# Performance work log

Measured on AMD Instinct MI355X. Metric: run time of the kernel, lower is better.

Reference implementation:

```python
import jax, jax.numpy as jnp
import numpy as np
import math

D_MODEL = 1024
NUM_HEADS = 16
HEAD_DIM = D_MODEL // NUM_HEADS
BATCH = 2
SEQ = 2048
THETA = 10000.0


def _rope_tables(seq_len, head_dim, theta=THETA):
    inv_freq = 1.0 / theta ** (jnp.arange(0, head_dim, 2, dtype=jnp.float32) / head_dim)
    pos = jnp.arange(seq_len, dtype=jnp.float32)
    freqs = jnp.outer(pos, inv_freq)                 # [S, hd/2]
    emb = jnp.concatenate([freqs, freqs], axis=-1)   # [S, hd]
    return jnp.cos(emb), jnp.sin(emb)


def _rotate_half(x):
    x1, x2 = jnp.split(x, 2, axis=-1)
    return jnp.concatenate([-x2, x1], axis=-1)


def setup_inputs() -> dict:
    key = jax.random.key(0)
    k1, k2, k3 = jax.random.split(key, 3)
    x = jax.random.normal(k1, (BATCH, SEQ, D_MODEL), dtype=jnp.float32)
    # causal mask: 1 where attend allowed, 0 where masked
    mask = jnp.tril(jnp.ones((SEQ, SEQ), dtype=jnp.int32))[None, None]
    w_qkv = jax.random.normal(k2, (D_MODEL, 3 * D_MODEL), dtype=jnp.float32) / math.sqrt(D_MODEL)
    w_out = jax.random.normal(k3, (D_MODEL, D_MODEL), dtype=jnp.float32) / math.sqrt(D_MODEL)
    return {"x": x, "mask": mask, "w_qkv": w_qkv, "w_out": w_out}


def reference(x, mask, w_qkv, w_out):
    B, S, _ = x.shape
    qkv = x @ w_qkv                                          # [B,S,3*D]
    qkv = qkv.reshape(B, S, 3, NUM_HEADS, HEAD_DIM)
    qkv = jnp.transpose(qkv, (2, 0, 3, 1, 4))                # [3,B,H,S,hd]
    q, k, v = qkv[0], qkv[1], qkv[2]
    cos, sin = _rope_tables(S, HEAD_DIM)                     # [S,hd]
    cos = cos[None, None]; sin = sin[None, None]
    q = q * cos + _rotate_half(q) * sin
    k = k * cos + _rotate_half(k) * sin
    scores = jnp.einsum('bhqd,bhkd->bhqk', q, k) / math.sqrt(HEAD_DIM)
    scores = jnp.where(mask == 0, -jnp.inf, scores)
    attn = jax.nn.softmax(scores, axis=-1)                   # dropout p=0 (eval)
    out = jnp.einsum('bhqk,bhkd->bhqd', attn, v)             # [B,H,S,hd]
    out = jnp.transpose(out, (0, 2, 1, 3)).reshape(B, S, D_MODEL)
    return out @ w_out
```

## Files before the change

kernel.cpp:

```cpp
#include <hip/hip_runtime.h>

typedef __bf16 bf16;
typedef __bf16 bf16x4 __attribute__((ext_vector_type(4)));
typedef __bf16 bf16x8 __attribute__((ext_vector_type(8)));
typedef short s16x4 __attribute__((ext_vector_type(4)));
typedef float f32x4 __attribute__((ext_vector_type(4)));

constexpr int BATCH = 2;
constexpr int SEQ   = 2048;
constexpr int DMODEL= 1024;
constexpr int NH    = 16;
constexpr int HD    = 64;
constexpr int M_ROWS= BATCH * SEQ;
constexpr int N_QKV = 3 * DMODEL;

__device__ __forceinline__ void gl_lds16(const bf16* g, bf16* l) {
  __builtin_amdgcn_global_load_lds(
      (const __attribute__((address_space(1))) unsigned int*)g,
      (__attribute__((address_space(3))) unsigned int*)l, 16, 0, 0);
}

__device__ __forceinline__ f32x4 mfma_16x16x16_bf16(bf16x4 a, bf16x4 b,
                                                    f32x4 c) {
#if defined(__HIP_DEVICE_COMPILE__)
  union { bf16x4 h; s16x4 s; } ua{a}, ub{b};
  return __builtin_amdgcn_mfma_f32_16x16x16bf16_1k(ua.s, ub.s, c, 0, 0, 0);
#else
  return c;
#endif
}

__global__ __launch_bounds__(256) void transpose_cast_kernel(
    const float* __restrict__ src, bf16* __restrict__ dst, int R, int C) {
  __shared__ float tile[32][33];
  const int c0 = blockIdx.x * 32, r0 = blockIdx.y * 32;
  const int tx = threadIdx.x, ty = threadIdx.y;
#pragma unroll
  for (int i = 0; i < 4; i++)
    tile[ty + 8 * i][tx] = src[(size_t)(r0 + ty + 8 * i) * C + c0 + tx];
  __syncthreads();
#pragma unroll
  for (int i = 0; i < 4; i++)
    dst[(size_t)(c0 + ty + 8 * i) * R + r0 + tx] = (bf16)tile[tx][ty + 8 * i];
}

__global__ __launch_bounds__(256) void cast_f32_bf16(
    const float* __restrict__ src, bf16* __restrict__ dst) {
  const int i = (blockIdx.x * 256 + threadIdx.x) * 8;
  float4 f0 = *(const float4*)&src[i];
  float4 f1 = *(const float4*)&src[i + 4];
  bf16x8 v;
  v[0] = (bf16)f0.x; v[1] = (bf16)f0.y; v[2] = (bf16)f0.z; v[3] = (bf16)f0.w;
  v[4] = (bf16)f1.x; v[5] = (bf16)f1.y; v[6] = (bf16)f1.z; v[7] = (bf16)f1.w;
  *(bf16x8*)&dst[i] = v;
}

#define GEMM_BODY(A, BT, K)                                                    \
  __shared__ bf16 As[128 * 32];                                                \
  __shared__ bf16 Bs[128 * 32];                                                \
  const int t = threadIdx.x;                                                   \
  const int m0 = blockIdx.y * 128;                                             \
  const int n0 = blockIdx.x * 128;                                             \
  const int w = t >> 6, lane = t & 63, g = lane >> 4, li = lane & 15;          \
  const int r0w = (w & 1) * 64, c0w = (w >> 1) * 64;                           \
  f32x4 acc[4][4] = {};                                                        \
  for (int k0 = 0; k0 < (K); k0 += 32) {                                       \
    __syncthreads();                                                           \
    _Pragma("unroll") for (int c = 0; c < 2; c++) {                            \
      const int idx = (w * 2 + c) * 64 + lane;                                 \
      const int row = idx >> 2, col = (idx & 3) * 8;                           \
      gl_lds16(&(A)[(size_t)(m0 + row) * (K) + k0 + col],                      \
               &As[(w * 2 + c) * 512]);                                        \
      gl_lds16(&(BT)[(size_t)(n0 + row) * (K) + k0 + col],                     \
               &Bs[(w * 2 + c) * 512]);                                        \
    }                                                                          \
    __syncthreads();                                                           \
    bf16x8 a[4], b[4];                                                         \
    _Pragma("unroll") for (int mt = 0; mt < 4; mt++)                           \
        a[mt] = *(const bf16x8*)&As[(r0w + mt * 16 + li) * 32 + g * 8];        \
    _Pragma("unroll") for (int nt = 0; nt < 4; nt++)                           \
        b[nt] = *(const bf16x8*)&Bs[(c0w + nt * 16 + li) * 32 + g * 8];        \
    _Pragma("unroll") for (int mt = 0; mt < 4; mt++)                           \
        _Pragma("unroll") for (int nt = 0; nt < 4; nt++)                       \
            acc[mt][nt] = __builtin_amdgcn_mfma_f32_16x16x32_bf16(             \
                a[mt], b[nt], acc[mt][nt], 0, 0, 0);                           \
  }

__global__ __launch_bounds__(256) void gemm_out64(
    const bf16* __restrict__ A, const bf16* __restrict__ BT,
    float* __restrict__ C, int M, int N, int K) {
  __shared__ bf16 As[64 * 32];
  __shared__ bf16 Bs[128 * 32];
  const int t = threadIdx.x;
  const int m0 = blockIdx.y * 64;
  const int n0 = blockIdx.x * 128;
  const int w = t >> 6, lane = t & 63, g = lane >> 4, li = lane & 15;
  const int r0w = (w & 1) * 32, c0w = (w >> 1) * 64;
  f32x4 acc[2][4] = {};
  for (int k0 = 0; k0 < K; k0 += 32) {
    __syncthreads();
    {
      const int idx = w * 64 + lane;
      const int row = idx >> 2, col = (idx & 3) * 8;
      gl_lds16(&A[(size_t)(m0 + row) * K + k0 + col], &As[w * 512]);
    }
#pragma unroll
    for (int c = 0; c < 2; c++) {
      const int idx = (w * 2 + c) * 64 + lane;
      const int row = idx >> 2, col = (idx & 3) * 8;
      gl_lds16(&BT[(size_t)(n0 + row) * K + k0 + col], &Bs[(w * 2 + c) * 512]);
    }
    __syncthreads();
    bf16x8 a[2], b[4];
#pragma unroll
    for (int mt = 0; mt < 2; mt++)
      a[mt] = *(const bf16x8*)&As[(r0w + mt * 16 + li) * 32 + g * 8];
#pragma unroll
    for (int nt = 0; nt < 4; nt++)
      b[nt] = *(const bf16x8*)&Bs[(c0w + nt * 16 + li) * 32 + g * 8];
#pragma unroll
    for (int mt = 0; mt < 2; mt++)
#pragma unroll
      for (int nt = 0; nt < 4; nt++)
        acc[mt][nt] = __builtin_amdgcn_mfma_f32_16x16x32_bf16(
            a[mt], b[nt], acc[mt][nt], 0, 0, 0);
  }
#pragma unroll
  for (int mt = 0; mt < 2; mt++)
#pragma unroll
    for (int nt = 0; nt < 4; nt++)
#pragma unroll
      for (int r = 0; r < 4; r++) {
        const int m = m0 + r0w + mt * 16 + g * 4 + r;
        const int n = n0 + c0w + nt * 16 + li;
        C[(size_t)m * N + n] = acc[mt][nt][r];
      }
}

__global__ __launch_bounds__(256) void gemm_qkv_rope(
    const bf16* __restrict__ A, const bf16* __restrict__ BT,
    bf16* __restrict__ Qb, bf16* __restrict__ Kb, bf16* __restrict__ Vt) {
  constexpr int K = DMODEL;
  GEMM_BODY(A, BT, K)

  const int region = n0 >> 10;
  const int b = m0 >> 11;
  const int h = ((n0 + c0w) >> 6) & 15;
  const size_t bh = (size_t)(b * NH + h);

  if (region < 2) {
    bf16* dst = region == 0 ? Qb : Kb;
    const float outsc = region == 0 ? 0.125f * 1.44269504f : 1.f;
    const float L = 13.287712379549449f;
    const float if0 = exp2f(-(float)(2 * li) / 64.f * L);
    const float if1 = exp2f(-(float)(2 * (li + 16)) / 64.f * L);
#pragma unroll
    for (int mt = 0; mt < 4; mt++)
#pragma unroll
      for (int r = 0; r < 4; r++) {
        const int s = (m0 + r0w + mt * 16 + g * 4 + r) & (SEQ - 1);
        float cs[2], sn[2];
        __sincosf((float)s * if0, &sn[0], &cs[0]);
        __sincosf((float)s * if1, &sn[1], &cs[1]);
#pragma unroll
        for (int nt = 0; nt < 4; nt++) {
          const int d = nt * 16 + li;
          const int par = nt & 1;
          const float a = acc[mt][nt][r];
          const float ap = acc[mt][nt ^ 2][r];
          const float v = (nt < 2) ? a * cs[par] - ap * sn[par]
                                   : a * cs[par] + ap * sn[par];
          dst[(bh * SEQ + s) * HD + d] = (bf16)(v * outsc);
        }
      }
  } else {
#pragma unroll
    for (int mt = 0; mt < 4; mt++)
#pragma unroll
      for (int nt = 0; nt < 4; nt++) {
        const int s = (m0 + r0w + mt * 16 + g * 4) & (SEQ - 1);
        const int d = nt * 16 + li;
        bf16x4 v;
#pragma unroll
        for (int r = 0; r < 4; r++) v[r] = (bf16)acc[mt][nt][r];
        *(bf16x4*)&Vt[(bh * HD + d) * SEQ + s] = v;
      }
  }
}

__global__ __launch_bounds__(256, 2) void flash_attn10(
    const bf16* __restrict__ Q, const bf16* __restrict__ Kb,
    const bf16* __restrict__ Vt, bf16* __restrict__ Oout) {
  const int bx = blockIdx.x;
  const int bh = bx & 31;
  const int pr = bx >> 5;
  const int t = threadIdx.x, w = t >> 6, lane = t & 63, g = lane >> 4,
            li = lane & 15;

  __shared__ bf16 Ks[2][4096];
  __shared__ bf16 Vs[2][4096];

  const bf16* Qh = Q  + (size_t)bh * SEQ * HD;
  const bf16* Kh = Kb + (size_t)bh * SEQ * HD;
  const bf16* Vh = Vt + (size_t)bh * HD * SEQ;
  const int b = bh >> 4, h = bh & 15;

  bf16x4 ones;
#pragma unroll
  for (int r = 0; r < 4; r++) ones[r] = (bf16)1.f;

  const int p0 = w * 128 + lane, p1 = p0 + 64;
  const int sr0 = p0 >> 3, sc0 = ((p0 & 7) ^ (sr0 & 7)) * 8;
  const int sr1 = p1 >> 3, sc1 = ((p1 & 7) ^ (sr1 & 7)) * 8;
  const int lo0 = w * 1024, lo1 = w * 1024 + 512;

  for (int seg = 0; seg < 2; seg++) {
    const int qt = seg ? 31 - pr : pr;
    const int q0 = qt * 64;
    const int qw = q0 + w * 16;
    const int jend = q0 + 64;

    bf16x8 qf[2];
#pragma unroll
    for (int ks = 0; ks < 2; ks++)
      qf[ks] = *(const bf16x8*)&Qh[(size_t)(qw + li) * HD + ks * 32 + g * 8];

    f32x4 o[4] = {};
    f32x4 o4  = {};

    gl_lds16(&Kh[(size_t)sr0 * HD + sc0], &Ks[0][lo0]);
    gl_lds16(&Kh[(size_t)sr1 * HD + sc1], &Ks[0][lo1]);
    gl_lds16(&Vh[(size_t)sr0 * SEQ + sc0], &Vs[0][lo0]);
    gl_lds16(&Vh[(size_t)sr1 * SEQ + sc1], &Vs[0][lo1]);
    __syncthreads();

    for (int j0 = 0; j0 < jend; j0 += 64) {
      const int cur = (j0 >> 6) & 1, nxt = cur ^ 1;
      if (j0 + 64 < jend) {
        const int jn = j0 + 64;
        gl_lds16(&Kh[(size_t)(jn + sr0) * HD + sc0], &Ks[nxt][lo0]);
        gl_lds16(&Kh[(size_t)(jn + sr1) * HD + sc1], &Ks[nxt][lo1]);
        gl_lds16(&Vh[(size_t)sr0 * SEQ + jn + sc0], &Vs[nxt][lo0]);
        gl_lds16(&Vh[(size_t)sr1 * SEQ + jn + sc1], &Vs[nxt][lo1]);
      }

      if (j0 <= qw + 15) {
        const bool masked = (j0 + 63 > qw);
        const int ntlim = min(4, ((qw + 15 - j0) >> 4) + 1);

        f32x4 sacc[4] = {};
#pragma unroll
        for (int ks = 0; ks < 2; ks++)
#pragma unroll
          for (int nt = 0; nt < 4; nt++) {
            if (nt >= ntlim) continue;
            const int rK = nt * 16 + li;
            const int pK = rK * 8 + ((ks * 4 + g) ^ (li & 7));
            bf16x8 kf = *(const bf16x8*)&Ks[cur][pK * 8];
            sacc[nt] = __builtin_amdgcn_mfma_f32_16x16x32_bf16(
                kf, qf[ks], sacc[nt], 0, 0, 0);
          }

        bf16x4 pf[4];
#pragma unroll
        for (int nt = 0; nt < 4; nt++) {
          if (nt >= ntlim) continue;
#pragma unroll
          for (int r = 0; r < 4; r++) {
            float v = sacc[nt][r];
            if (masked) {
              const int kk = j0 + nt * 16 + g * 4 + r;
              v = (kk <= qw + li) ? v : -1e30f;
            }
            pf[nt][r] = (bf16)exp2f(v);
          }
        }

#pragma unroll
        for (int nt = 0; nt < 4; nt++) {
          if (nt >= ntlim) continue;
          o4 = mfma_16x16x16_bf16(ones, pf[nt], o4);
#pragma unroll
          for (int dt = 0; dt < 4; dt++) {
            const int rV = dt * 16 + li;
            const int cg = nt * 2 + (g >> 1);
            const int pV = rV * 8 + (cg ^ (rV & 7));
            bf16x4 vfrag = *(const bf16x4*)&Vs[cur][pV * 8 + (g & 1) * 4];
            o[dt] = mfma_16x16x16_bf16(vfrag, pf[nt], o[dt]);
          }
        }
      }
      __syncthreads();
    }

    const float inv_l = 1.f / o4[0];
    const int s = qw + li;
#pragma unroll
    for (int dt = 0; dt < 4; dt++) {
      bf16x4 ov;
#pragma unroll
      for (int r = 0; r < 4; r++) ov[r] = (bf16)(o[dt][r] * inv_l);
      *(bf16x4*)&Oout[((size_t)(b * SEQ + s)) * DMODEL + h * 64 + dt * 16 +
                      g * 4] = ov;
    }
  }
}

extern "C" void kernel_launch(void* const* d_in, const int* in_sizes, int n_in,
                              void* d_out, int out_size, void* d_ws,
                              size_t ws_size, hipStream_t stream) {
  const float* x     = (const float*)d_in[0];
  const float* w_qkv = (const float*)d_in[2];
  const float* w_out = (const float*)d_in[3];
  float* out = (float*)d_out;

  char* ws = (char*)d_ws;
  bf16* WqkvT = (bf16*)(ws);
  bf16* WoutT = (bf16*)(ws + 6291456);
  bf16* xb    = (bf16*)(ws + 8388608);
  bf16* Qb    = (bf16*)(ws + 16777216);
  bf16* Kbuf  = (bf16*)(ws + 25165824);
  bf16* Vt    = (bf16*)(ws + 33554432);
  bf16* attn  = (bf16*)(ws + 41943040);

  cast_f32_bf16<<<M_ROWS * DMODEL / 2048, 256, 0, stream>>>(x, xb);
  transpose_cast_kernel<<<dim3(N_QKV / 32, DMODEL / 32), dim3(32, 8), 0,
                          stream>>>(w_qkv, WqkvT, DMODEL, N_QKV);
  transpose_cast_kernel<<<dim3(DMODEL / 32, DMODEL / 32), dim3(32, 8), 0,
                          stream>>>(w_out, WoutT, DMODEL, DMODEL);
  gemm_qkv_rope<<<dim3(N_QKV / 128, M_ROWS / 128), 256, 0, stream>>>(
      xb, WqkvT, Qb, Kbuf, Vt);
  flash_attn10<<<dim3(512), 256, 0, stream>>>(Qb, Kbuf, Vt, attn);
  gemm_out64<<<dim3(DMODEL / 128, M_ROWS / 64), 256, 0, stream>>>(
      attn, WoutT, out, M_ROWS, DMODEL, DMODEL);
}
```

Baseline: 221.5 us.

## Split paired causal q-tiles into separate blocks with 32-key tiles

The attention kernel no longer pairs a light and a heavy query tile per block. It launches one block per query tile, with the heaviest tiles scheduled first, and halves the K/V tile to 32 keys so each tile needs half the shared memory. Launch bounds rise to allow six blocks per CU. The aim is more parallelism and occupancy with dynamic load balancing, at the cost of more barriers per key and Q loads that are no longer amortised across two segments.

```diff
diff --git a/kernel.cpp b/kernel.cpp
--- a/kernel.cpp
+++ b/kernel.cpp
@@ -188,121 +188,114 @@
   }
 }
 
-__global__ __launch_bounds__(256, 2) void flash_attn10(
+__global__ __launch_bounds__(256, 6) void flash_attn11(
     const bf16* __restrict__ Q, const bf16* __restrict__ Kb,
     const bf16* __restrict__ Vt, bf16* __restrict__ Oout) {
   const int bx = blockIdx.x;
+  const int qt = 31 - (bx >> 5);
   const int bh = bx & 31;
-  const int pr = bx >> 5;
+  const int q0 = qt * 64;
   const int t = threadIdx.x, w = t >> 6, lane = t & 63, g = lane >> 4,
             li = lane & 15;
 
-  __shared__ bf16 Ks[2][4096];
-  __shared__ bf16 Vs[2][4096];
+  __shared__ bf16 Ks[2][2048];
+  __shared__ bf16 Vs[2][2048];
 
   const bf16* Qh = Q  + (size_t)bh * SEQ * HD;
   const bf16* Kh = Kb + (size_t)bh * SEQ * HD;
   const bf16* Vh = Vt + (size_t)bh * HD * SEQ;
+
+  const int qw = q0 + w * 16;
+
+  bf16x8 qf[2];
+#pragma unroll
+  for (int ks = 0; ks < 2; ks++)
+    qf[ks] = *(const bf16x8*)&Qh[(size_t)(qw + li) * HD + ks * 32 + g * 8];
+
+  f32x4 o[4] = {};
+  f32x4 o4  = {};
+  bf16x4 ones;
+#pragma unroll
+  for (int r = 0; r < 4; r++) ones[r] = (bf16)1.f;
+
+  const int krow = t >> 3, kcol = ((t & 7) ^ (krow & 7)) * 8;
+  const int vrow = t >> 2, vcol = ((t & 3) ^ (vrow & 3)) * 8;
+  const int lo = w * 512;
+
+  const int jend = q0 + 64;
+
+  gl_lds16(&Kh[(size_t)krow * HD + kcol], &Ks[0][lo]);
+  gl_lds16(&Vh[(size_t)vrow * SEQ + vcol], &Vs[0][lo]);
+  __syncthreads();
+
+  for (int j0 = 0; j0 < jend; j0 += 32) {
+    const int cur = (j0 >> 5) & 1, nxt = cur ^ 1;
+    if (j0 + 32 < jend) {
+      const int jn = j0 + 32;
+      gl_lds16(&Kh[(size_t)(jn + krow) * HD + kcol], &Ks[nxt][lo]);
+      gl_lds16(&Vh[(size_t)vrow * SEQ + jn + vcol], &Vs[nxt][lo]);
+    }
+
+    if (j0 <= qw + 15) {
+      const bool masked = (j0 + 31 > qw);
+      const int ntlim = min(2, ((qw + 15 - j0) >> 4) + 1);
+
+      f32x4 sacc[2] = {};
+#pragma unroll
+      for (int ks = 0; ks < 2; ks++)
+#pragma unroll
+        for (int nt = 0; nt < 2; nt++) {
+          if (nt >= ntlim) continue;
+          const int rK = nt * 16 + li;
+          const int pK = rK * 8 + ((ks * 4 + g) ^ (rK & 7));
+          bf16x8 kf = *(const bf16x8*)&Ks[cur][pK * 8];
+          sacc[nt] = __builtin_amdgcn_mfma_f32_16x16x32_bf16(kf, qf[ks],
+                                                             sacc[nt], 0, 0, 0);
+        }
+
+      bf16x4 pf[2];
+#pragma unroll
+      for (int nt = 0; nt < 2; nt++) {
+        if (nt >= ntlim) continue;
+#pragma unroll
+        for (int r = 0; r < 4; r++) {
+          float v = sacc[nt][r];
+          if (masked) {
+            const int kk = j0 + nt * 16 + g * 4 + r;
+            v = (kk <= qw + li) ? v : -1e30f;
+          }
+          pf[nt][r] = (bf16)exp2f(v);
+        }
+      }
+
+#pragma unroll
+      for (int nt = 0; nt < 2; nt++) {
+        if (nt >= ntlim) continue;
+        o4 = mfma_16x16x16_bf16(ones, pf[nt], o4);
+#pragma unroll
+        for (int dt = 0; dt < 4; dt++) {
+          const int rV = dt * 16 + li;
+          const int cgv = nt * 2 + (g >> 1);
+          const int pV = rV * 4 + (cgv ^ (rV & 3));
+          bf16x4 vfrag = *(const bf16x4*)&Vs[cur][pV * 8 + (g & 1) * 4];
+          o[dt] = mfma_16x16x16_bf16(vfrag, pf[nt], o[dt]);
+        }
+      }
+    }
+    __syncthreads();
+  }
+
+  const float inv_l = 1.f / o4[0];
+
   const int b = bh >> 4, h = bh & 15;
-
-  bf16x4 ones;
-#pragma unroll
-  for (int r = 0; r < 4; r++) ones[r] = (bf16)1.f;
-
-  const int p0 = w * 128 + lane, p1 = p0 + 64;
-  const int sr0 = p0 >> 3, sc0 = ((p0 & 7) ^ (sr0 & 7)) * 8;
-  const int sr1 = p1 >> 3, sc1 = ((p1 & 7) ^ (sr1 & 7)) * 8;
-  const int lo0 = w * 1024, lo1 = w * 1024 + 512;
-
-  for (int seg = 0; seg < 2; seg++) {
-    const int qt = seg ? 31 - pr : pr;
-    const int q0 = qt * 64;
-    const int qw = q0 + w * 16;
-    const int jend = q0 + 64;
-
-    bf16x8 qf[2];
-#pragma unroll
-    for (int ks = 0; ks < 2; ks++)
-      qf[ks] = *(const bf16x8*)&Qh[(size_t)(qw + li) * HD + ks * 32 + g * 8];
-
-    f32x4 o[4] = {};
-    f32x4 o4  = {};
-
-    gl_lds16(&Kh[(size_t)sr0 * HD + sc0], &Ks[0][lo0]);
-    gl_lds16(&Kh[(size_t)sr1 * HD + sc1], &Ks[0][lo1]);
-    gl_lds16(&Vh[(size_t)sr0 * SEQ + sc0], &Vs[0][lo0]);
-    gl_lds16(&Vh[(size_t)sr1 * SEQ + sc1], &Vs[0][lo1]);
-    __syncthreads();
-
-    for (int j0 = 0; j0 < jend; j0 += 64) {
-      const int cur = (j0 >> 6) & 1, nxt = cur ^ 1;
-      if (j0 + 64 < jend) {
-        const int jn = j0 + 64;
-        gl_lds16(&Kh[(size_t)(jn + sr0) * HD + sc0], &Ks[nxt][lo0]);
-        gl_lds16(&Kh[(size_t)(jn + sr1) * HD + sc1], &Ks[nxt][lo1]);
-        gl_lds16(&Vh[(size_t)sr0 * SEQ + jn + sc0], &Vs[nxt][lo0]);
-        gl_lds16(&Vh[(size_t)sr1 * SEQ + jn + sc1], &Vs[nxt][lo1]);
-      }
-
-      if (j0 <= qw + 15) {
-        const bool masked = (j0 + 63 > qw);
-        const int ntlim = min(4, ((qw + 15 - j0) >> 4) + 1);
-
-        f32x4 sacc[4] = {};
-#pragma unroll
-        for (int ks = 0; ks < 2; ks++)
-#pragma unroll
-          for (int nt = 0; nt < 4; nt++) {
-            if (nt >= ntlim) continue;
-            const int rK = nt * 16 + li;
-            const int pK = rK * 8 + ((ks * 4 + g) ^ (li & 7));
-            bf16x8 kf = *(const bf16x8*)&Ks[cur][pK * 8];
-            sacc[nt] = __builtin_amdgcn_mfma_f32_16x16x32_bf16(
-                kf, qf[ks], sacc[nt], 0, 0, 0);
-          }
-
-        bf16x4 pf[4];
-#pragma unroll
-        for (int nt = 0; nt < 4; nt++) {
-          if (nt >= ntlim) continue;
-#pragma unroll
-          for (int r = 0; r < 4; r++) {
-            float v = sacc[nt][r];
-            if (masked) {
-              const int kk = j0 + nt * 16 + g * 4 + r;
-              v = (kk <= qw + li) ? v : -1e30f;
-            }
-            pf[nt][r] = (bf16)exp2f(v);
-          }
-        }
-
-#pragma unroll
-        for (int nt = 0; nt < 4; nt++) {
-          if (nt >= ntlim) continue;
-          o4 = mfma_16x16x16_bf16(ones, pf[nt], o4);
-#pragma unroll
-          for (int dt = 0; dt < 4; dt++) {
-            const int rV = dt * 16 + li;
-            const int cg = nt * 2 + (g >> 1);
-            const int pV = rV * 8 + (cg ^ (rV & 7));
-            bf16x4 vfrag = *(const bf16x4*)&Vs[cur][pV * 8 + (g & 1) * 4];
-            o[dt] = mfma_16x16x16_bf16(vfrag, pf[nt], o[dt]);
-          }
-        }
-      }
-      __syncthreads();
-    }
-
-    const float inv_l = 1.f / o4[0];
-    const int s = qw + li;
-#pragma unroll
-    for (int dt = 0; dt < 4; dt++) {
-      bf16x4 ov;
-#pragma unroll
-      for (int r = 0; r < 4; r++) ov[r] = (bf16)(o[dt][r] * inv_l);
-      *(bf16x4*)&Oout[((size_t)(b * SEQ + s)) * DMODEL + h * 64 + dt * 16 +
-                      g * 4] = ov;
-    }
+  const int s = qw + li;
+#pragma unroll
+  for (int dt = 0; dt < 4; dt++) {
+    bf16x4 ov;
+#pragma unroll
+    for (int r = 0; r < 4; r++) ov[r] = (bf16)(o[dt][r] * inv_l);
+    *(bf16x4*)&Oout[((size_t)(b * SEQ + s)) * DMODEL + h * 64 + dt * 16 +
+                    g * 4] = ov;
   }
 }
 
@@ -330,7 +323,7 @@
                           stream>>>(w_out, WoutT, DMODEL, DMODEL);
   gemm_qkv_rope<<<dim3(N_QKV / 128, M_ROWS / 128), 256, 0, stream>>>(
       xb, WqkvT, Qb, Kbuf, Vt);
-  flash_attn10<<<dim3(512), 256, 0, stream>>>(Qb, Kbuf, Vt, attn);
+  flash_attn11<<<dim3(1024), 256, 0, stream>>>(Qb, Kbuf, Vt, attn);
   gemm_out64<<<dim3(DMODEL / 128, M_ROWS / 64), 256, 0, stream>>>(
       attn, WoutT, out, M_ROWS, DMODEL, DMODEL);
 }
```

Measured after the change: 220.2 us. About the same (-0.6%).
